# Performance work log

Measured on AMD Instinct MI355X. Metric: run time of the kernel, lower is better.

Reference implementation:

```python
import jax, jax.numpy as jnp
import numpy as np

QUERY_SIZE = 1024
MEMORY_SIZE = 1024
ATTN_SIZE = 512
B, T = 64, 2048


def setup_inputs() -> dict:
    key = jax.random.key(0)
    k1, k2, k3, k4, k5 = jax.random.split(key, 5)
    query = jax.random.normal(k1, (B, QUERY_SIZE), dtype=jnp.float32)
    memory = jax.random.normal(k2, (B, T, MEMORY_SIZE), dtype=jnp.float32)
    # nn.Linear weights: shape (out_features, in_features); y = x @ W.T
    s_q = 1.0 / np.sqrt(QUERY_SIZE)
    s_m = 1.0 / np.sqrt(MEMORY_SIZE)
    s_v = 1.0 / np.sqrt(ATTN_SIZE)
    W_query = jax.random.uniform(k3, (ATTN_SIZE, QUERY_SIZE), jnp.float32, -s_q, s_q)
    W_memory = jax.random.uniform(k4, (ATTN_SIZE, MEMORY_SIZE), jnp.float32, -s_m, s_m)
    W_v = jax.random.uniform(k5, (1, ATTN_SIZE), jnp.float32, -s_v, s_v)
    return {"query": query, "memory": memory, "W_query": W_query,
            "W_memory": W_memory, "W_v": W_v}


def reference(query, memory, W_query, W_memory, W_v):
    # w_query: [B, A]; w_memory: [B, T, A]
    w_query = query @ W_query.T
    w_memory = jnp.einsum("btm,am->bta", memory, W_memory)
    # additive score: v^T tanh(wq + wm) -> [B, T]
    scores = jnp.einsum("bta,a->bt", jnp.tanh(w_query[:, None, :] + w_memory), W_v[0])
    alpha = jax.nn.softmax(scores, axis=-1)  # [B, T]
    # context = alpha @ memory -> [B, 1, M]
    context = jnp.einsum("bt,btm->bm", alpha, memory)[:, None, :]
    return (alpha, context)
```

## Files before the change

### kernel.cpp

```cpp
#include <hip/hip_runtime.h>
#include <hip/hip_bf16.h>
#include <cstdint>
#include <cstddef>

#define Bn 64
#define Tn 2048
#define Mn 1024
#define An 512
#define Qn 1024

#define RT 64
#define BK 32
#define NKC (Mn / BK)

typedef __attribute__((ext_vector_type(8))) short short8;
typedef __attribute__((ext_vector_type(4))) float f32x4;
typedef __attribute__((ext_vector_type(2))) float f32x2;
typedef __attribute__((ext_vector_type(4))) unsigned short us4;

static __device__ __forceinline__ unsigned short f2bf(float f) {
  uint32_t u = __float_as_uint(f);
  u += 0x7fff + ((u >> 16) & 1);
  return (unsigned short)(u >> 16);
}

static __device__ __forceinline__ void gl_lds16(const void* g, void* l) {
  __builtin_amdgcn_global_load_lds(
      (const __attribute__((address_space(1))) unsigned int*)g,
      (__attribute__((address_space(3))) unsigned int*)l, 16, 0, 0);
}

__global__ void zero_kernel(float* __restrict__ ctx, float* __restrict__ Zacc) {
  int i = blockIdx.x * 256 + threadIdx.x;
  if (i < Bn * Mn) ctx[i] = 0.0f;
  else if (i < Bn * Mn + Bn) Zacc[i - Bn * Mn] = 0.0f;
}

__global__ void cvt_wm_kernel(const float* __restrict__ Wm, unsigned short* __restrict__ out) {
  int i = blockIdx.x * 256 + threadIdx.x;
  if (i < An * Mn) out[i] = f2bf(Wm[i]);
}

__global__ void wq_kernel(const float* __restrict__ query, const float* __restrict__ Wq,
                          float* __restrict__ wqout) {
  __shared__ __align__(16) float qs[Qn];
  const int b = blockIdx.x >> 2;
  const int ag = blockIdx.x & 3;
  const int tid = threadIdx.x;
  for (int i = tid; i < Qn; i += 128) qs[i] = query[b * Qn + i];
  __syncthreads();
  const int a = ag * 128 + tid;
  const f32x4* w = (const f32x4*)(Wq + (size_t)a * Qn);
  const f32x4* q4 = (const f32x4*)qs;
  float acc = 0.f;
#pragma unroll 8
  for (int m = 0; m < Qn / 4; ++m) {
    f32x4 wv = w[m];
    f32x4 qv = q4[m];
    acc += wv.x * qv.x + wv.y * qv.y + wv.z * qv.z + wv.w * qv.w;
  }
  wqout[b * An + a] = acc;
}

__launch_bounds__(512, 4)
__global__ void fused_kernel(const float* __restrict__ mem,
                             const float* __restrict__ wq,
                             const unsigned short* __restrict__ Wmb,
                             const float* __restrict__ Wv,
                             float* __restrict__ out,
                             float* __restrict__ Zacc) {
  __shared__ __align__(16) unsigned short As[2][RT * BK];
  __shared__ __align__(16) unsigned short Bs[2][An * BK];
  __shared__ float s_score[RT];
  __shared__ float s_e[RT];

  const int tid = threadIdx.x;
  const int b  = blockIdx.x & (Bn - 1);
  const int tt = blockIdx.x >> 6;
  const int t0 = tt * RT;

  const int lane = tid & 63;
  const int w = tid >> 6;
  const int l15 = lane & 15;
  const int quad = lane >> 4;

  if (tid < RT) s_score[tid] = 0.f;

  const int arow = tid >> 3;
  const int ah = tid & 7;
  const float* asrc = mem + ((size_t)(b * Tn + t0 + arow)) * Mn + ah * 4;
  const int au = ((ah >> 1) + (arow >> 1)) & 3;
  const int aoff = arow * BK + au * 8 + (ah & 1) * 4;

  const int ba0 = w * 64 + (lane >> 2);
  const int bj = lane & 3;

  int aro[4], bro[4];
#pragma unroll
  for (int rt = 0; rt < 4; ++rt) {
    int row = rt * 16 + l15;
    aro[rt] = row * BK + (((quad + (row >> 1)) & 3) * 8);
  }
#pragma unroll
  for (int ct = 0; ct < 4; ++ct) {
    int a = w * 64 + ct * 16 + l15;
    bro[ct] = a * BK + (((quad + (a >> 1)) & 3) * 8);
  }

  f32x4 av = *(const f32x4*)asrc;
  {
    us4 o; o.x = f2bf(av.x); o.y = f2bf(av.y); o.z = f2bf(av.z); o.w = f2bf(av.w);
    *(us4*)&As[0][aoff] = o;
  }
#pragma unroll
  for (int i = 0; i < 4; ++i) {
    int a = ba0 + i * 16;
    int q = (bj - (a >> 1)) & 3;
    gl_lds16(Wmb + (size_t)a * Mn + q * 8, &Bs[0][(size_t)(w * 4 + i) * 512]);
  }
  __syncthreads();

  f32x4 acc[4][4] = {};

  for (int kc = 0; kc < NKC; ++kc) {
    const int p = kc & 1, np = p ^ 1;
    if (kc + 1 < NKC) {
      av = *(const f32x4*)(asrc + (kc + 1) * BK);
#pragma unroll
      for (int i = 0; i < 4; ++i) {
        int a = ba0 + i * 16;
        int q = (bj - (a >> 1)) & 3;
        gl_lds16(Wmb + (size_t)a * Mn + (kc + 1) * BK + q * 8,
                 &Bs[np][(size_t)(w * 4 + i) * 512]);
      }
    }

    short8 af[4], bf[4];
#pragma unroll
    for (int i = 0; i < 4; ++i) af[i] = *(const short8*)&As[p][aro[i]];
#pragma unroll
    for (int i = 0; i < 4; ++i) bf[i] = *(const short8*)&Bs[p][bro[i]];

#pragma unroll
    for (int rt = 0; rt < 4; ++rt)
#pragma unroll
      for (int ct = 0; ct < 4; ++ct)
        acc[rt][ct] = __builtin_amdgcn_mfma_f32_16x16x32_bf16(af[rt], bf[ct], acc[rt][ct], 0, 0, 0);

    if (kc + 1 < NKC) {
      us4 o; o.x = f2bf(av.x); o.y = f2bf(av.y); o.z = f2bf(av.z); o.w = f2bf(av.w);
      *(us4*)&As[np][aoff] = o;
    }
    __syncthreads();
  }

  const float* wqb = wq + b * An;
  {
    float rs[4][4];
#pragma unroll
    for (int rt = 0; rt < 4; ++rt)
#pragma unroll
      for (int g = 0; g < 4; ++g) rs[rt][g] = 0.f;

#pragma unroll
    for (int ct = 0; ct < 4; ++ct) {
      const int a = w * 64 + ct * 16 + l15;
      const float wqa = wqb[a];
      const float va = Wv[a];
#pragma unroll
      for (int rt = 0; rt < 4; ++rt) {
#pragma unroll
        for (int g = 0; g < 4; ++g) {
          float x = wqa + acc[rt][ct][g];
          float ez = __expf(2.0f * x);
          float th = 1.0f - 2.0f * __builtin_amdgcn_rcpf(ez + 1.0f);
          rs[rt][g] += va * th;
        }
      }
    }
#pragma unroll
    for (int rt = 0; rt < 4; ++rt) {
#pragma unroll
      for (int g = 0; g < 4; ++g) {
        float v = rs[rt][g];
        v += __shfl_xor(v, 1);
        v += __shfl_xor(v, 2);
        v += __shfl_xor(v, 4);
        v += __shfl_xor(v, 8);
        if (l15 == 0) atomicAdd(&s_score[rt * 16 + quad * 4 + g], v);
      }
    }
  }
  __syncthreads();

  if (tid < RT) {
    float e = __expf(s_score[tid]);
    s_e[tid] = e;
    out[(size_t)b * Tn + t0 + tid] = e;
    float z = e;
    z += __shfl_xor(z, 1);
    z += __shfl_xor(z, 2);
    z += __shfl_xor(z, 4);
    z += __shfl_xor(z, 8);
    z += __shfl_xor(z, 16);
    z += __shfl_xor(z, 32);
    if (lane == 0) atomicAdd(&Zacc[b], z);
  }
  __syncthreads();

  {
    const float* mrow = mem + ((size_t)(b * Tn + t0)) * Mn + 2 * tid;
    float c0 = 0.f, c1 = 0.f;
#pragma unroll 8
    for (int r = 0; r < RT; ++r) {
      f32x2 v = *(const f32x2*)(mrow + (size_t)r * Mn);
      float e = s_e[r];
      c0 += e * v.x;
      c1 += e * v.y;
    }
    float* ctx = out + Bn * Tn + (size_t)b * Mn + 2 * tid;
    atomicAdd(&ctx[0], c0);
    atomicAdd(&ctx[1], c1);
  }
}

__global__ void finalize_kernel(float* __restrict__ out, const float* __restrict__ Zacc) {
  int i = blockIdx.x * 256 + threadIdx.x;
  if (i < Bn * Tn) {
    int b = i >> 11;
    out[i] /= Zacc[b];
  } else if (i < Bn * Tn + Bn * Mn) {
    int j = i - Bn * Tn;
    int b = j >> 10;
    out[i] /= Zacc[b];
  }
}

extern "C" void kernel_launch(void* const* d_in, const int* in_sizes, int n_in,
                              void* d_out, int out_size, void* d_ws, size_t ws_size,
                              hipStream_t stream) {
  const float* query    = (const float*)d_in[0];
  const float* memory   = (const float*)d_in[1];
  const float* W_query  = (const float*)d_in[2];
  const float* W_memory = (const float*)d_in[3];
  const float* W_v      = (const float*)d_in[4];
  float* out = (float*)d_out;

  float* wq = (float*)d_ws;
  unsigned short* Wmb = (unsigned short*)((char*)d_ws + (size_t)Bn * An * 4);
  float* Zacc = (float*)((char*)d_ws + (size_t)Bn * An * 4 + (size_t)An * Mn * 2);

  zero_kernel<<<(Bn * Mn + Bn + 255) / 256, 256, 0, stream>>>(out + Bn * Tn, Zacc);
  cvt_wm_kernel<<<(An * Mn + 255) / 256, 256, 0, stream>>>(W_memory, Wmb);
  wq_kernel<<<Bn * 4, 128, 0, stream>>>(query, W_query, wq);
  fused_kernel<<<Bn * (Tn / RT), 512, 0, stream>>>(memory, wq, Wmb, W_v, out, Zacc);
  finalize_kernel<<<(Bn * Tn + Bn * Mn + 255) / 256, 256, 0, stream>>>(out, Zacc);
}
```

Measured before the change: 902.0 us.

## Double row tile and deepen B-operand pipeline with explicit waitcnt barriers

```diff
diff --git a/kernel.cpp b/kernel.cpp
--- a/kernel.cpp
+++ b/kernel.cpp
@@ -9,11 +9,12 @@
 #define An 512
 #define Qn 1024
 
-#define RT 64
+#define RT 128
 #define BK 32
 #define NKC (Mn / BK)
 
 typedef __attribute__((ext_vector_type(8))) short short8;
+typedef __attribute__((ext_vector_type(8))) unsigned short us8;
 typedef __attribute__((ext_vector_type(4))) float f32x4;
 typedef __attribute__((ext_vector_type(2))) float f32x2;
 typedef __attribute__((ext_vector_type(4))) unsigned short us4;
@@ -62,7 +63,18 @@
   wqout[b * An + a] = acc;
 }
 
-__launch_bounds__(512, 4)
+static __device__ __forceinline__ void stage_b(const unsigned short* __restrict__ Wmb,
+                                               unsigned short* dst,
+                                               int ba0, int bj, int k) {
+#pragma unroll
+  for (int i = 0; i < 4; ++i) {
+    int a = ba0 + i * 16;
+    int q = (bj - (a >> 1)) & 3;
+    gl_lds16(Wmb + (size_t)a * Mn + (size_t)k * BK + q * 8, dst + (size_t)i * 512);
+  }
+}
+
+__launch_bounds__(512, 2)
 __global__ void fused_kernel(const float* __restrict__ mem,
                              const float* __restrict__ wq,
                              const unsigned short* __restrict__ Wmb,
@@ -70,7 +82,7 @@
                              float* __restrict__ out,
                              float* __restrict__ Zacc) {
   __shared__ __align__(16) unsigned short As[2][RT * BK];
-  __shared__ __align__(16) unsigned short Bs[2][An * BK];
+  __shared__ __align__(16) unsigned short Bs[4][An * BK];
   __shared__ float s_score[RT];
   __shared__ float s_e[RT];
 
@@ -86,18 +98,17 @@
 
   if (tid < RT) s_score[tid] = 0.f;
 
-  const int arow = tid >> 3;
-  const int ah = tid & 7;
-  const float* asrc = mem + ((size_t)(b * Tn + t0 + arow)) * Mn + ah * 4;
-  const int au = ((ah >> 1) + (arow >> 1)) & 3;
-  const int aoff = arow * BK + au * 8 + (ah & 1) * 4;
+  const int arow = tid >> 2;
+  const int ah = tid & 3;
+  const f32x4* ap = (const f32x4*)(mem + ((size_t)(b * Tn + t0 + arow)) * Mn) + ah * 2;
+  const int aoff = arow * BK + (((ah + (arow >> 1)) & 3) * 8);
 
   const int ba0 = w * 64 + (lane >> 2);
   const int bj = lane & 3;
 
-  int aro[4], bro[4];
-#pragma unroll
-  for (int rt = 0; rt < 4; ++rt) {
+  int aro[8], bro[4];
+#pragma unroll
+  for (int rt = 0; rt < 8; ++rt) {
     int row = rt * 16 + l15;
     aro[rt] = row * BK + (((quad + (row >> 1)) & 3) * 8);
   }
@@ -107,58 +118,71 @@
     bro[ct] = a * BK + (((quad + (a >> 1)) & 3) * 8);
   }
 
-  f32x4 av = *(const f32x4*)asrc;
+  f32x4 av[2][2];
+
+  av[0][0] = ap[0];  av[0][1] = ap[1];
+  stage_b(Wmb, &Bs[0][w * 2048], ba0, bj, 0);
+  av[1][0] = ap[8];  av[1][1] = ap[9];
+  stage_b(Wmb, &Bs[1][w * 2048], ba0, bj, 1);
   {
-    us4 o; o.x = f2bf(av.x); o.y = f2bf(av.y); o.z = f2bf(av.z); o.w = f2bf(av.w);
-    *(us4*)&As[0][aoff] = o;
-  }
-#pragma unroll
-  for (int i = 0; i < 4; ++i) {
-    int a = ba0 + i * 16;
-    int q = (bj - (a >> 1)) & 3;
-    gl_lds16(Wmb + (size_t)a * Mn + q * 8, &Bs[0][(size_t)(w * 4 + i) * 512]);
-  }
-  __syncthreads();
-
-  f32x4 acc[4][4] = {};
-
-  for (int kc = 0; kc < NKC; ++kc) {
-    const int p = kc & 1, np = p ^ 1;
-    if (kc + 1 < NKC) {
-      av = *(const f32x4*)(asrc + (kc + 1) * BK);
-#pragma unroll
-      for (int i = 0; i < 4; ++i) {
-        int a = ba0 + i * 16;
-        int q = (bj - (a >> 1)) & 3;
-        gl_lds16(Wmb + (size_t)a * Mn + (kc + 1) * BK + q * 8,
-                 &Bs[np][(size_t)(w * 4 + i) * 512]);
-      }
-    }
-
-    short8 af[4], bf[4];
-#pragma unroll
-    for (int i = 0; i < 4; ++i) af[i] = *(const short8*)&As[p][aro[i]];
-#pragma unroll
-    for (int i = 0; i < 4; ++i) bf[i] = *(const short8*)&Bs[p][bro[i]];
-
-#pragma unroll
-    for (int rt = 0; rt < 4; ++rt)
-#pragma unroll
-      for (int ct = 0; ct < 4; ++ct)
-        acc[rt][ct] = __builtin_amdgcn_mfma_f32_16x16x32_bf16(af[rt], bf[ct], acc[rt][ct], 0, 0, 0);
-
-    if (kc + 1 < NKC) {
-      us4 o; o.x = f2bf(av.x); o.y = f2bf(av.y); o.z = f2bf(av.z); o.w = f2bf(av.w);
-      *(us4*)&As[np][aoff] = o;
-    }
-    __syncthreads();
+    us8 o;
+    o[0] = (unsigned short)f2bf(av[0][0].x); o[1] = (unsigned short)f2bf(av[0][0].y);
+    o[2] = (unsigned short)f2bf(av[0][0].z); o[3] = (unsigned short)f2bf(av[0][0].w);
+    o[4] = (unsigned short)f2bf(av[0][1].x); o[5] = (unsigned short)f2bf(av[0][1].y);
+    o[6] = (unsigned short)f2bf(av[0][1].z); o[7] = (unsigned short)f2bf(av[0][1].w);
+    *(us8*)&As[0][aoff] = o;
+  }
+  asm volatile("s_waitcnt lgkmcnt(0)" ::: "memory");
+  __builtin_amdgcn_sched_barrier(0);
+  __builtin_amdgcn_s_barrier();
+  __builtin_amdgcn_sched_barrier(0);
+
+  f32x4 acc[8][4] = {};
+
+  for (int kk = 0; kk < NKC; kk += 4) {
+#pragma unroll
+    for (int j = 0; j < 4; ++j) {
+      const int kc = kk + j;
+      int k2 = kc + 2; if (k2 > NKC - 1) k2 = NKC - 1;
+
+      av[j & 1][0] = ap[(size_t)k2 * 8];
+      av[j & 1][1] = ap[(size_t)k2 * 8 + 1];
+      stage_b(Wmb, &Bs[(j + 2) & 3][w * 2048], ba0, bj, k2);
+
+      asm volatile("s_waitcnt vmcnt(12)" ::: "memory");
+
+      short8 bfv[4];
+#pragma unroll
+      for (int i = 0; i < 4; ++i) bfv[i] = *(const short8*)&Bs[j][bro[i]];
+#pragma unroll
+      for (int rt = 0; rt < 8; ++rt) {
+        short8 afr = *(const short8*)&As[j & 1][aro[rt]];
+#pragma unroll
+        for (int ct = 0; ct < 4; ++ct)
+          acc[rt][ct] = __builtin_amdgcn_mfma_f32_16x16x32_bf16(afr, bfv[ct], acc[rt][ct], 0, 0, 0);
+      }
+
+      {
+        f32x4 a0 = av[(j + 1) & 1][0], a1 = av[(j + 1) & 1][1];
+        us8 o;
+        o[0] = (unsigned short)f2bf(a0.x); o[1] = (unsigned short)f2bf(a0.y);
+        o[2] = (unsigned short)f2bf(a0.z); o[3] = (unsigned short)f2bf(a0.w);
+        o[4] = (unsigned short)f2bf(a1.x); o[5] = (unsigned short)f2bf(a1.y);
+        o[6] = (unsigned short)f2bf(a1.z); o[7] = (unsigned short)f2bf(a1.w);
+        *(us8*)&As[(j + 1) & 1][aoff] = o;
+      }
+      asm volatile("s_waitcnt lgkmcnt(0)" ::: "memory");
+      __builtin_amdgcn_sched_barrier(0);
+      __builtin_amdgcn_s_barrier();
+      __builtin_amdgcn_sched_barrier(0);
+    }
   }
 
   const float* wqb = wq + b * An;
   {
-    float rs[4][4];
-#pragma unroll
-    for (int rt = 0; rt < 4; ++rt)
+    float rs[8][4];
+#pragma unroll
+    for (int rt = 0; rt < 8; ++rt)
 #pragma unroll
       for (int g = 0; g < 4; ++g) rs[rt][g] = 0.f;
 
@@ -168,7 +192,7 @@
       const float wqa = wqb[a];
       const float va = Wv[a];
 #pragma unroll
-      for (int rt = 0; rt < 4; ++rt) {
+      for (int rt = 0; rt < 8; ++rt) {
 #pragma unroll
         for (int g = 0; g < 4; ++g) {
           float x = wqa + acc[rt][ct][g];
@@ -179,7 +203,7 @@
       }
     }
 #pragma unroll
-    for (int rt = 0; rt < 4; ++rt) {
+    for (int rt = 0; rt < 8; ++rt) {
 #pragma unroll
       for (int g = 0; g < 4; ++g) {
         float v = rs[rt][g];
@@ -211,7 +235,7 @@
   {
     const float* mrow = mem + ((size_t)(b * Tn + t0)) * Mn + 2 * tid;
     float c0 = 0.f, c1 = 0.f;
-#pragma unroll 8
+#pragma unroll 16
     for (int r = 0; r < RT; ++r) {
       f32x2 v = *(const f32x2*)(mrow + (size_t)r * Mn);
       float e = s_e[r];
```

After: 933.6 us. +3.5%, slower.

## Load W_memory fragments directly from global in MFMA-ready layout, drop LDS B tile

Applied to the files above, without the earlier changes.

```diff
diff --git a/kernel.cpp b/kernel.cpp
--- a/kernel.cpp
+++ b/kernel.cpp
@@ -14,6 +14,7 @@
 #define NKC (Mn / BK)
 
 typedef __attribute__((ext_vector_type(8))) short short8;
+typedef __attribute__((ext_vector_type(8))) unsigned short us8;
 typedef __attribute__((ext_vector_type(4))) float f32x4;
 typedef __attribute__((ext_vector_type(2))) float f32x2;
 typedef __attribute__((ext_vector_type(4))) unsigned short us4;
@@ -24,12 +25,6 @@
   return (unsigned short)(u >> 16);
 }
 
-static __device__ __forceinline__ void gl_lds16(const void* g, void* l) {
-  __builtin_amdgcn_global_load_lds(
-      (const __attribute__((address_space(1))) unsigned int*)g,
-      (__attribute__((address_space(3))) unsigned int*)l, 16, 0, 0);
-}
-
 __global__ void zero_kernel(float* __restrict__ ctx, float* __restrict__ Zacc) {
   int i = blockIdx.x * 256 + threadIdx.x;
   if (i < Bn * Mn) ctx[i] = 0.0f;
@@ -37,8 +32,18 @@
 }
 
 __global__ void cvt_wm_kernel(const float* __restrict__ Wm, unsigned short* __restrict__ out) {
-  int i = blockIdx.x * 256 + threadIdx.x;
-  if (i < An * Mn) out[i] = f2bf(Wm[i]);
+  int t = blockIdx.x * 256 + threadIdx.x;
+  if (t >= (An * Mn) / 8) return;
+  int kc  = t >> 11;
+  int ab  = (t >> 6) & 31;
+  int lane = t & 63;
+  int row = ab * 16 + (lane & 15);
+  int col = kc * 32 + (lane >> 4) * 8;
+  const float* src = Wm + (size_t)row * Mn + col;
+  us8 o;
+#pragma unroll
+  for (int e = 0; e < 8; ++e) o[e] = f2bf(src[e]);
+  *(us8*)(out + (size_t)t * 8) = o;
 }
 
 __global__ void wq_kernel(const float* __restrict__ query, const float* __restrict__ Wq,
@@ -70,7 +75,6 @@
                              float* __restrict__ out,
                              float* __restrict__ Zacc) {
   __shared__ __align__(16) unsigned short As[2][RT * BK];
-  __shared__ __align__(16) unsigned short Bs[2][An * BK];
   __shared__ float s_score[RT];
   __shared__ float s_e[RT];
 
@@ -92,66 +96,57 @@
   const int au = ((ah >> 1) + (arow >> 1)) & 3;
   const int aoff = arow * BK + au * 8 + (ah & 1) * 4;
 
-  const int ba0 = w * 64 + (lane >> 2);
-  const int bj = lane & 3;
-
-  int aro[4], bro[4];
+  int aro[4];
 #pragma unroll
   for (int rt = 0; rt < 4; ++rt) {
     int row = rt * 16 + l15;
     aro[rt] = row * BK + (((quad + (row >> 1)) & 3) * 8);
   }
-#pragma unroll
-  for (int ct = 0; ct < 4; ++ct) {
-    int a = w * 64 + ct * 16 + l15;
-    bro[ct] = a * BK + (((quad + (a >> 1)) & 3) * 8);
-  }
-
-  f32x4 av = *(const f32x4*)asrc;
+
+  const short8* bp = (const short8*)Wmb;
+  const int bbase = (w * 4) * 64 + lane;
+
+  f32x4 av[2];
+  av[0] = *(const f32x4*)asrc;
+  av[1] = *(const f32x4*)(asrc + BK);
   {
-    us4 o; o.x = f2bf(av.x); o.y = f2bf(av.y); o.z = f2bf(av.z); o.w = f2bf(av.w);
+    us4 o; o.x = f2bf(av[0].x); o.y = f2bf(av[0].y); o.z = f2bf(av[0].z); o.w = f2bf(av[0].w);
     *(us4*)&As[0][aoff] = o;
   }
-#pragma unroll
-  for (int i = 0; i < 4; ++i) {
-    int a = ba0 + i * 16;
-    int q = (bj - (a >> 1)) & 3;
-    gl_lds16(Wmb + (size_t)a * Mn + q * 8, &Bs[0][(size_t)(w * 4 + i) * 512]);
-  }
-  __syncthreads();
+  asm volatile("s_waitcnt lgkmcnt(0)" ::: "memory");
+  __builtin_amdgcn_sched_barrier(0);
+  __builtin_amdgcn_s_barrier();
+  __builtin_amdgcn_sched_barrier(0);
 
   f32x4 acc[4][4] = {};
 
+#pragma unroll 2
   for (int kc = 0; kc < NKC; ++kc) {
-    const int p = kc & 1, np = p ^ 1;
+    if (kc + 2 < NKC) av[kc & 1] = *(const f32x4*)(asrc + (size_t)(kc + 2) * BK);
+
+    short8 bfv[4];
+#pragma unroll
+    for (int ct = 0; ct < 4; ++ct) bfv[ct] = bp[bbase + kc * 2048 + ct * 64];
+
+    short8 af[4];
+#pragma unroll
+    for (int i = 0; i < 4; ++i) af[i] = *(const short8*)&As[kc & 1][aro[i]];
+
+#pragma unroll
+    for (int rt = 0; rt < 4; ++rt)
+#pragma unroll
+      for (int ct = 0; ct < 4; ++ct)
+        acc[rt][ct] = __builtin_amdgcn_mfma_f32_16x16x32_bf16(af[rt], bfv[ct], acc[rt][ct], 0, 0, 0);
+
     if (kc + 1 < NKC) {
-      av = *(const f32x4*)(asrc + (kc + 1) * BK);
-#pragma unroll
-      for (int i = 0; i < 4; ++i) {
-        int a = ba0 + i * 16;
-        int q = (bj - (a >> 1)) & 3;
-        gl_lds16(Wmb + (size_t)a * Mn + (kc + 1) * BK + q * 8,
-                 &Bs[np][(size_t)(w * 4 + i) * 512]);
-      }
-    }
-
-    short8 af[4], bf[4];
-#pragma unroll
-    for (int i = 0; i < 4; ++i) af[i] = *(const short8*)&As[p][aro[i]];
-#pragma unroll
-    for (int i = 0; i < 4; ++i) bf[i] = *(const short8*)&Bs[p][bro[i]];
-
-#pragma unroll
-    for (int rt = 0; rt < 4; ++rt)
-#pragma unroll
-      for (int ct = 0; ct < 4; ++ct)
-        acc[rt][ct] = __builtin_amdgcn_mfma_f32_16x16x32_bf16(af[rt], bf[ct], acc[rt][ct], 0, 0, 0);
-
-    if (kc + 1 < NKC) {
-      us4 o; o.x = f2bf(av.x); o.y = f2bf(av.y); o.z = f2bf(av.z); o.w = f2bf(av.w);
-      *(us4*)&As[np][aoff] = o;
-    }
-    __syncthreads();
+      f32x4 a = av[(kc + 1) & 1];
+      us4 o; o.x = f2bf(a.x); o.y = f2bf(a.y); o.z = f2bf(a.z); o.w = f2bf(a.w);
+      *(us4*)&As[(kc + 1) & 1][aoff] = o;
+    }
+    asm volatile("s_waitcnt lgkmcnt(0)" ::: "memory");
+    __builtin_amdgcn_sched_barrier(0);
+    __builtin_amdgcn_s_barrier();
+    __builtin_amdgcn_sched_barrier(0);
   }
 
   const float* wqb = wq + b * An;
@@ -251,7 +246,7 @@
   float* Zacc = (float*)((char*)d_ws + (size_t)Bn * An * 4 + (size_t)An * Mn * 2);
 
   zero_kernel<<<(Bn * Mn + Bn + 255) / 256, 256, 0, stream>>>(out + Bn * Tn, Zacc);
-  cvt_wm_kernel<<<(An * Mn + 255) / 256, 256, 0, stream>>>(W_memory, Wmb);
+  cvt_wm_kernel<<<(An * Mn / 8 + 255) / 256, 256, 0, stream>>>(W_memory, Wmb);
   wq_kernel<<<Bn * 4, 128, 0, stream>>>(query, W_query, wq);
   fused_kernel<<<Bn * (Tn / RT), 512, 0, stream>>>(memory, wq, Wmb, W_v, out, Zacc);
   finalize_kernel<<<(Bn * Tn + Bn * Mn + 255) / 256, 256, 0, stream>>>(out, Zacc);
```

Result: faster. 880.0 us (-2.4%).
